# Optimization experiments

Measured on AMD Instinct MI355X. Metric: run time of the kernel, lower is better.

The kernel has to match this reference:

```python
import jax, jax.numpy as jnp
import numpy as np

SCALE = 1.0 / np.sqrt(64.0)  # hard-coded 64**0.5 in original, independent of dims


def setup_inputs() -> dict:
    key = jax.random.key(0)
    k1, k2 = jax.random.split(key)
    x = jax.random.normal(k1, (8, 2048, 1024), dtype=jnp.float32)
    # kernel[0]=W_Q, kernel[1]=W_K, kernel[2]=W_V, each [d_in, d_out]
    kernel = jax.random.normal(k2, (3, 1024, 1024), dtype=jnp.float32) * 0.02
    return {"x": x, "kernel": kernel}


def reference(x, kernel):
    # x: [b, s, d_in], kernel: [3, d_in, d_out]
    wq = jnp.einsum('bsd,de->bse', x, kernel[0])
    wk = jnp.einsum('bsd,de->bse', x, kernel[1])
    wv = jnp.einsum('bsd,de->bse', x, kernel[2])
    scores = jnp.einsum('bqe,bke->bqk', wq, wk) * SCALE  # [b, s, s]
    attn = jax.nn.softmax(scores, axis=-1)
    return jnp.einsum('bqk,bke->bqe', attn, wv)  # [b, s, d_out]
```

## Files before the change

kernel.cpp:

```cpp
#include <hip/hip_runtime.h>
#include <stdint.h>

typedef unsigned short u16;
typedef unsigned short u16x4 __attribute__((ext_vector_type(4)));
typedef unsigned short u16x8 __attribute__((ext_vector_type(8)));
typedef _Float16 f16x8 __attribute__((ext_vector_type(8)));
typedef float f32x4 __attribute__((ext_vector_type(4)));

__device__ __forceinline__ u16 f2h(float f) {
  _Float16 x = (_Float16)f;
  return __builtin_bit_cast(u16, x);
}

__device__ __forceinline__ void gld16(const void* g, void* l) {
  __builtin_amdgcn_global_load_lds(
      (const __attribute__((address_space(1))) unsigned int*)g,
      (__attribute__((address_space(3))) unsigned int*)l,
      16, 0, 0);
}

#define BAR __builtin_amdgcn_s_barrier()
#define SCHEDB __builtin_amdgcn_sched_barrier(0)
#define LGKM0                                        \
  do {                                               \
    asm volatile("s_waitcnt lgkmcnt(0)" ::: "memory"); \
    __builtin_amdgcn_sched_barrier(0);               \
  } while (0)
#define LGKM8 asm volatile("s_waitcnt lgkmcnt(8)" ::: "memory")
#define VM6 asm volatile("s_waitcnt vmcnt(6)" ::: "memory")
#define VM0 asm volatile("s_waitcnt vmcnt(0)" ::: "memory")

#define TBM 256
#define TBN 256
#define TBK 64

template <int QM, int QN>
__device__ __forceinline__ void mfma_quad(f32x4 (&acc)[8][4],
                                          const f16x8 (&ar)[4][2],
                                          const f16x8 (&br)[2][2]) {
#pragma unroll
  for (int kk = 0; kk < 2; ++kk)
#pragma unroll
    for (int mm = 0; mm < 4; ++mm)
#pragma unroll
      for (int nn = 0; nn < 2; ++nn)
        acc[QM * 4 + mm][QN * 2 + nn] = __builtin_amdgcn_mfma_f32_16x16x32_f16(
            ar[mm][kk], br[nn][kk], acc[QM * 4 + mm][QN * 2 + nn], 0, 0, 0);
}

template <int EPI, int XSWZ>
__global__ __launch_bounds__(512, 2) void gemm256(
    const u16* __restrict__ Ap, const u16* __restrict__ Bp,
    void* __restrict__ Cp, float* __restrict__ xtra, int K, int lda, int ldb,
    int ldc, long sA, long sB, long sC) {
  __shared__ char lds[131072];

  const int gx = gridDim.x, gy = gridDim.y;
  int bx, by, z;
  if constexpr (XSWZ == 1) {
    const int p = (blockIdx.z * gy + blockIdx.y) * gx + blockIdx.x;
    z = p & 7;
    const int rest = p >> 3;
    bx = rest % gx;
    by = rest / gx;
  } else {
    const int lin = (blockIdx.z * gy + blockIdx.y) * gx + blockIdx.x;
    const int cpx = (gx * gy * gridDim.z) >> 3;
    const int swz = (lin & 7) * cpx + (lin >> 3);
    bx = swz % gx;
    const int tq = swz / gx;
    by = tq % gy;
    z = tq / gy;
  }

  const int tid = threadIdx.x;
  const int lane = tid & 63, wid = tid >> 6;
  const int wr = wid >> 2, wc = wid & 3;
  const int l15 = lane & 15, l4 = lane >> 4;
  const int bm = by * TBM, bn = bx * TBN;

  const u16* Ag = Ap + (long)z * sA + (long)bm * lda;
  const u16* Bg = Bp + (long)z * sB + (long)bn * ldb;

  const int sw = l15 & 7;
  const int s0 = (l4 ^ sw) * 16, s1 = ((4 + l4) ^ sw) * 16;
  int aB[2][2], bB[2][2];
  aB[0][0] = wr * 16384 + l15 * 128 + s0;
  aB[0][1] = wr * 16384 + l15 * 128 + s1;
  bB[0][0] = 32768 + (wc >> 1) * 16384 + ((wc & 1) * 64 + l15) * 128 + s0;
  bB[0][1] = 32768 + (wc >> 1) * 16384 + ((wc & 1) * 64 + l15) * 128 + s1;
  aB[1][0] = aB[0][0] + 65536;
  aB[1][1] = aB[0][1] + 65536;
  bB[1][0] = bB[0][0] + 65536;
  bB[1][1] = bB[0][1] + 65536;

#define DSA(BUF, QM, AR)                                                     \
  do {                                                                       \
    _Pragma("unroll") for (int mm = 0; mm < 4; ++mm) {                       \
      AR[mm][0] = *(const f16x8*)(lds + aB[BUF][0] + (QM)*8192 + mm * 2048); \
      AR[mm][1] = *(const f16x8*)(lds + aB[BUF][1] + (QM)*8192 + mm * 2048); \
    }                                                                        \
  } while (0)
#define DSB(BUF, QN, BR)                                                     \
  do {                                                                       \
    _Pragma("unroll") for (int nn = 0; nn < 2; ++nn) {                       \
      BR[nn][0] = *(const f16x8*)(lds + bB[BUF][0] + (QN)*4096 + nn * 2048); \
      BR[nn][1] = *(const f16x8*)(lds + bB[BUF][1] + (QN)*4096 + nn * 2048); \
    }                                                                        \
  } while (0)

  const u16 *gpA0[2], *gpA1[2], *gpB0[2], *gpB1[2];
  int loA0[2], loA1[2], loB0[2], loB1[2];
  {
    const u16* bases[4] = {Ag, Ag + 128L * lda, Bg, Bg + 128L * ldb};
    const int lds_[4] = {lda, lda, ldb, ldb};
    const u16** gps[4] = {gpA0, gpA1, gpB0, gpB1};
    int* los[4] = {loA0, loA1, loB0, loB1};
#pragma unroll
    for (int X = 0; X < 4; ++X)
#pragma unroll
      for (int it = 0; it < 2; ++it) {
        int idx = it * 512 + tid, r = idx >> 3, p = idx & 7, s = p ^ (r & 7);
        gps[X][it] = bases[X] + (long)r * lds_[X] + s * 8;
        los[X][it] = X * 16384 + (it * 512 + wid * 64) * 16;
      }
  }
#define STAGE(X, BUF, kt)                                              \
  do {                                                                 \
    long ko = (long)(kt) << 7;                                         \
    gld16((const char*)gp##X[0] + ko, lds + ((BUF)*65536 + lo##X[0])); \
    gld16((const char*)gp##X[1] + ko, lds + ((BUF)*65536 + lo##X[1])); \
  } while (0)

  f32x4 acc[8][4] = {};
  f16x8 a0[4][2], a1[4][2], b0[2][2], b1[2][2];
  const int nk = K / TBK;

  STAGE(A0, 0, 0);
  STAGE(A1, 0, 0);
  STAGE(B0, 0, 0);
  STAGE(B1, 0, 0);
  STAGE(A0, 1, 1);
  STAGE(A1, 1, 1);
  STAGE(B0, 1, 1);
  VM6;
  BAR;
  SCHEDB;

#define TILE(BUF, t)                                                 \
  do {                                                               \
                       \
    DSA(BUF, 0, a0);                                                 \
    DSB(BUF, 0, b0);                                                 \
    if ((t) + 1 < nk) STAGE(B1, BUF ^ 1, (t) + 1);                   \
    LGKM8;                                                           \
    BAR;                                                             \
    LGKM0;                                                           \
    __builtin_amdgcn_s_setprio(1);                                   \
    mfma_quad<0, 0>(acc, a0, b0);                                    \
    __builtin_amdgcn_s_setprio(0);                                   \
    SCHEDB;                                                          \
    BAR;                                                             \
                           \
    DSA(BUF, 1, a1);                                                 \
    if ((t) + 2 < nk) STAGE(A0, BUF, (t) + 2);                       \
    BAR;                                                             \
    LGKM0;                                                           \
    __builtin_amdgcn_s_setprio(1);                                   \
    mfma_quad<1, 0>(acc, a1, b0);                                    \
    __builtin_amdgcn_s_setprio(0);                                   \
    SCHEDB;                                                          \
    BAR;                                                             \
                           \
    DSB(BUF, 1, b1);                                                 \
    if ((t) + 2 < nk) STAGE(A1, BUF, (t) + 2);                       \
    BAR;                                                             \
    LGKM0;                                                           \
    __builtin_amdgcn_s_setprio(1);                                   \
    mfma_quad<0, 1>(acc, a0, b1);                                    \
    __builtin_amdgcn_s_setprio(0);                                   \
    SCHEDB;                                                          \
    BAR;                                                             \
     \
    if ((t) + 2 < nk) {                                              \
      STAGE(B0, BUF, (t) + 2);                                       \
      VM6;                                                           \
    } else if ((t) + 1 < nk) {                                       \
      VM0;                                                           \
    }                                                                \
    BAR;                                                             \
    __builtin_amdgcn_s_setprio(1);                                   \
    mfma_quad<1, 1>(acc, a1, b1);                                    \
    __builtin_amdgcn_s_setprio(0);                                   \
    SCHEDB;                                                          \
    BAR;                                                             \
  } while (0)

  for (int t = 0; t < nk; t += 2) {
    TILE(0, t);
    TILE(1, t + 1);
  }

  if constexpr (EPI == 0) {
    if (bn < 2048) {
      u16* C = (u16*)Cp;
#pragma unroll
      for (int m = 0; m < 8; ++m)
#pragma unroll
        for (int n = 0; n < 4; ++n) {
          int row = bm + wr * 128 + m * 16 + l4 * 4;
          int col = bn + wc * 64 + n * 16 + l15;
#pragma unroll
          for (int r = 0; r < 4; ++r)
            C[(long)(row + r) * ldc + col] = f2h(acc[m][n][r]);
        }
    } else {
#pragma unroll
      for (int m = 0; m < 8; ++m) {
        const int slotk = wr * 16 + m * 2 + (l4 >> 1);
        const int koff8 = (l4 & 1) * 8;
#pragma unroll
        for (int n = 0; n < 4; ++n) {
          const int e = wc * 64 + n * 16 + l15;
          u16x4 pk;
#pragma unroll
          for (int rr = 0; rr < 4; ++rr) pk[rr] = f2h(acc[m][n][rr]);
          *(u16x4*)(lds + e * 512 + ((slotk ^ (e & 31)) << 4) + koff8) = pk;
        }
      }
      __syncthreads();
      u16* Vt = (u16*)xtra;
      const int zz = bm >> 11;
      const int kb = bm & 2047;
      const int e = tid >> 1;
      const int c2 = (tid & 1) * 16;
      u16* dst = Vt + (long)zz * 2097152 + (long)((bn - 2048) + e) * 2048 + kb;
      const char* src = lds + e * 512;
      const int ex = e & 31;
#pragma unroll
      for (int j = 0; j < 16; ++j) {
        const int c = c2 + j;
        u16x8 v = *(const u16x8*)(src + ((c ^ ex) << 4));
        *(u16x8*)(dst + c * 8) = v;
      }
    }
  } else if constexpr (EPI == 1) {
    u16* C = (u16*)Cp + (long)z * sC;
    float* rp = (float*)lds;
#pragma unroll
    for (int m = 0; m < 8; ++m) {
#pragma unroll
      for (int r = 0; r < 4; ++r) {
        const int row = bm + wr * 128 + m * 16 + l4 * 4 + r;
        float ps = 0.f;
#pragma unroll
        for (int n = 0; n < 4; ++n) {
          float p = __expf(acc[m][n][r] * 0.125f - 3.0f);
          C[(long)row * ldc + bn + wc * 64 + n * 16 + l15] = f2h(p);
          ps += p;
        }
#pragma unroll
        for (int d = 1; d < 16; d <<= 1) ps += __shfl_xor(ps, d, 64);
        if (l15 == 0) rp[wc * 256 + wr * 128 + m * 16 + l4 * 4 + r] = ps;
      }
    }
    __syncthreads();
    if (tid < 256) {
      float s = rp[tid] + rp[256 + tid] + rp[512 + tid] + rp[768 + tid];
      xtra[((long)z * 2048 + bm + tid) * 8 + bx] = s;
    }
  } else {
    float* C = (float*)Cp + (long)z * sC;
    float* ivl = (float*)lds;
    if (tid < 256) ivl[tid] = xtra[(long)z * 2048 + bm + tid];
    __syncthreads();
#pragma unroll
    for (int m = 0; m < 8; ++m)
#pragma unroll
      for (int r = 0; r < 4; ++r) {
        const int rloc = wr * 128 + m * 16 + l4 * 4 + r;
        const float iv = ivl[rloc];
        const long row = bm + rloc;
#pragma unroll
        for (int n = 0; n < 4; ++n)
          C[row * ldc + bn + wc * 64 + n * 16 + l15] = acc[m][n][r] * iv;
      }
  }
#undef TILE
#undef STAGE
#undef DSA
#undef DSB
}

__global__ __launch_bounds__(256) void rowinv_k(const float* __restrict__ Spart,
                                                float* __restrict__ rowinv) {
  const int i = blockIdx.x * 256 + threadIdx.x;
  const float* p = Spart + (long)i * 8;
  float s = 0.f;
#pragma unroll
  for (int j = 0; j < 8; ++j) s += p[j];
  rowinv[i] = 1.0f / s;
}

__global__ __launch_bounds__(256) void transpose_f32_to_f16(
    const float* __restrict__ in, u16* __restrict__ out, int R, int C,
    int ldin, long sIn, long sOut) {
  __shared__ u16 T[64][72];
  const long bi = blockIdx.z;
  const float* ip = in + bi * sIn;
  u16* op = out + bi * sOut;
  const int r0 = blockIdx.y * 64, c0 = blockIdx.x * 64;
  const int t = threadIdx.x, c8 = t & 7, rr = t >> 3;
#pragma unroll
  for (int h = 0; h < 2; ++h) {
    const int r = rr + h * 32;
    const float* g = ip + (long)(r0 + r) * ldin + c0 + c8 * 8;
    float4 a = *(const float4*)g;
    float4 b = *(const float4*)(g + 4);
    u16x8 v;
    v[0] = f2h(a.x); v[1] = f2h(a.y); v[2] = f2h(a.z); v[3] = f2h(a.w);
    v[4] = f2h(b.x); v[5] = f2h(b.y); v[6] = f2h(b.z); v[7] = f2h(b.w);
    *(u16x8*)&T[r][c8 * 8] = v;
  }
  __syncthreads();
#pragma unroll
  for (int h = 0; h < 2; ++h) {
    const int oc = rr + h * 32;
    u16x8 v;
#pragma unroll
    for (int j = 0; j < 8; ++j) v[j] = T[c8 * 8 + j][oc];
    *(u16x8*)(op + (long)(c0 + oc) * R + r0 + c8 * 8) = v;
  }
}

__global__ __launch_bounds__(256) void f32_to_f16(const float* __restrict__ in,
                                                  u16* __restrict__ out,
                                                  long n8) {
  long i = (long)blockIdx.x * 256 + threadIdx.x;
  const long stride = (long)gridDim.x * 256;
  for (; i < n8; i += stride) {
    const float* g = in + i * 8;
    float4 a = *(const float4*)g;
    float4 b = *(const float4*)(g + 4);
    u16x8 o;
    o[0] = f2h(a.x); o[1] = f2h(a.y); o[2] = f2h(a.z); o[3] = f2h(a.w);
    o[4] = f2h(b.x); o[5] = f2h(b.y); o[6] = f2h(b.z); o[7] = f2h(b.w);
    *(u16x8*)(out + i * 8) = o;
  }
}

extern "C" void kernel_launch(void* const* d_in, const int* in_sizes, int n_in,
                              void* d_out, int out_size, void* d_ws,
                              size_t ws_size, hipStream_t stream) {
  const float* x = (const float*)d_in[0];
  const float* w = (const float*)d_in[1];
  float* out = (float*)d_out;

  u16* ws = (u16*)d_ws;
  u16* QKV = ws;
  u16* Wt = ws + 50331648L;
  float* Spart = (float*)(ws + 50331648L);
  float* rowinv = (float*)(ws + 50593792L);
  u16* Vt = ws + 53477376L;
  u16* xh = ws + 70254592L;
  u16* S = ws + 70254592L;

  f32_to_f16<<<2048, 256, 0, stream>>>(x, xh, 2097152L);

  transpose_f32_to_f16<<<dim3(16, 16, 3), 256, 0, stream>>>(
      w, Wt, 1024, 1024, 1024, 1048576L, 1048576L);

  gemm256<0, 0><<<dim3(12, 64, 1), 512, 0, stream>>>(
      xh, Wt, (void*)QKV, (float*)Vt, 1024, 1024, 1024, 3072, 0L, 0L, 0L);

  gemm256<1, 1><<<dim3(8, 8, 8), 512, 0, stream>>>(
      QKV, QKV + 1024, (void*)S, Spart, 1024, 3072, 3072, 2048, 6291456L,
      6291456L, 4194304L);

  rowinv_k<<<dim3(64), 256, 0, stream>>>(Spart, rowinv);

  gemm256<2, 1><<<dim3(4, 8, 8), 512, 0, stream>>>(
      S, Vt, (void*)out, rowinv, 2048, 2048, 2048, 1024, 4194304L, 2097152L,
      2097152L);
}
```

Measured before the change: 280.4 us.

## Merge prep kernels, fold row-inverse into final GEMM, reshape V-transpose stores

Merges the x f32-to-f16 cast and the weight transpose into one launch, and removes the separate rowinv kernel by having the final GEMM epilogue sum the eight partial row sums and take the reciprocal itself. It also changes the thread-to-data mapping of the V transpose writeback so that eight consecutive threads write contiguous 16-byte chunks of a row, giving more coalesced global stores. The aim is to cut two kernel launches and their gaps, plus improve store coalescing. In exchange, every final-GEMM block now recomputes the row inverses redundantly.

```diff
diff --git a/kernel.cpp b/kernel.cpp
--- a/kernel.cpp
+++ b/kernel.cpp
@@ -232,16 +232,21 @@
       u16* Vt = (u16*)xtra;
       const int zz = bm >> 11;
       const int kb = bm & 2047;
-      const int e = tid >> 1;
-      const int c2 = (tid & 1) * 16;
-      u16* dst = Vt + (long)zz * 2097152 + (long)((bn - 2048) + e) * 2048 + kb;
-      const char* src = lds + e * 512;
-      const int ex = e & 31;
-#pragma unroll
-      for (int j = 0; j < 16; ++j) {
-        const int c = c2 + j;
-        u16x8 v = *(const u16x8*)(src + ((c ^ ex) << 4));
-        *(u16x8*)(dst + c * 8) = v;
+      const int er = tid >> 3;
+      const int q = tid & 7;
+#pragma unroll
+      for (int p = 0; p < 4; ++p) {
+        const int e = p * 64 + er;
+        const char* src = lds + e * 512;
+        u16* dst =
+            Vt + (long)zz * 2097152 + (long)((bn - 2048) + e) * 2048 + kb;
+        const int ex = e & 31;
+#pragma unroll
+        for (int j = 0; j < 4; ++j) {
+          const int c = q + 8 * j;
+          u16x8 v = *(const u16x8*)(src + ((c ^ ex) << 4));
+          *(u16x8*)(dst + c * 8) = v;
+        }
       }
     }
   } else if constexpr (EPI == 1) {
@@ -272,7 +277,13 @@
   } else {
     float* C = (float*)Cp + (long)z * sC;
     float* ivl = (float*)lds;
-    if (tid < 256) ivl[tid] = xtra[(long)z * 2048 + bm + tid];
+    if (tid < 256) {
+      const float* sp = xtra + ((long)z * 2048 + bm + tid) * 8;
+      float s = 0.f;
+#pragma unroll
+      for (int j = 0; j < 8; ++j) s += sp[j];
+      ivl[tid] = 1.0f / s;
+    }
     __syncthreads();
 #pragma unroll
     for (int m = 0; m < 8; ++m)
@@ -292,60 +303,50 @@
 #undef DSB
 }
 
-__global__ __launch_bounds__(256) void rowinv_k(const float* __restrict__ Spart,
-                                                float* __restrict__ rowinv) {
-  const int i = blockIdx.x * 256 + threadIdx.x;
-  const float* p = Spart + (long)i * 8;
-  float s = 0.f;
-#pragma unroll
-  for (int j = 0; j < 8; ++j) s += p[j];
-  rowinv[i] = 1.0f / s;
-}
-
-__global__ __launch_bounds__(256) void transpose_f32_to_f16(
-    const float* __restrict__ in, u16* __restrict__ out, int R, int C,
-    int ldin, long sIn, long sOut) {
-  __shared__ u16 T[64][72];
-  const long bi = blockIdx.z;
-  const float* ip = in + bi * sIn;
-  u16* op = out + bi * sOut;
-  const int r0 = blockIdx.y * 64, c0 = blockIdx.x * 64;
-  const int t = threadIdx.x, c8 = t & 7, rr = t >> 3;
-#pragma unroll
-  for (int h = 0; h < 2; ++h) {
-    const int r = rr + h * 32;
-    const float* g = ip + (long)(r0 + r) * ldin + c0 + c8 * 8;
-    float4 a = *(const float4*)g;
-    float4 b = *(const float4*)(g + 4);
-    u16x8 v;
-    v[0] = f2h(a.x); v[1] = f2h(a.y); v[2] = f2h(a.z); v[3] = f2h(a.w);
-    v[4] = f2h(b.x); v[5] = f2h(b.y); v[6] = f2h(b.z); v[7] = f2h(b.w);
-    *(u16x8*)&T[r][c8 * 8] = v;
-  }
-  __syncthreads();
-#pragma unroll
-  for (int h = 0; h < 2; ++h) {
-    const int oc = rr + h * 32;
-    u16x8 v;
-#pragma unroll
-    for (int j = 0; j < 8; ++j) v[j] = T[c8 * 8 + j][oc];
-    *(u16x8*)(op + (long)(c0 + oc) * R + r0 + c8 * 8) = v;
-  }
-}
-
-__global__ __launch_bounds__(256) void f32_to_f16(const float* __restrict__ in,
-                                                  u16* __restrict__ out,
-                                                  long n8) {
-  long i = (long)blockIdx.x * 256 + threadIdx.x;
-  const long stride = (long)gridDim.x * 256;
-  for (; i < n8; i += stride) {
-    const float* g = in + i * 8;
-    float4 a = *(const float4*)g;
-    float4 b = *(const float4*)(g + 4);
-    u16x8 o;
-    o[0] = f2h(a.x); o[1] = f2h(a.y); o[2] = f2h(a.z); o[3] = f2h(a.w);
-    o[4] = f2h(b.x); o[5] = f2h(b.y); o[6] = f2h(b.z); o[7] = f2h(b.w);
-    *(u16x8*)(out + i * 8) = o;
+__global__ __launch_bounds__(256) void prep(const float* __restrict__ x,
+                                            const float* __restrict__ w,
+                                            u16* __restrict__ xh,
+                                            u16* __restrict__ Wt) {
+  const int b = blockIdx.x;
+  if (b < 768) {
+    __shared__ u16 T[64][72];
+    const int z = b >> 8, rem = b & 255, by = rem >> 4, bxx = rem & 15;
+    const float* ip = w + (long)z * 1048576;
+    u16* op = Wt + (long)z * 1048576;
+    const int r0 = by * 64, c0 = bxx * 64;
+    const int t = threadIdx.x, c8 = t & 7, rr = t >> 3;
+#pragma unroll
+    for (int h = 0; h < 2; ++h) {
+      const int r = rr + h * 32;
+      const float* g = ip + (long)(r0 + r) * 1024 + c0 + c8 * 8;
+      float4 a = *(const float4*)g;
+      float4 bb = *(const float4*)(g + 4);
+      u16x8 v;
+      v[0] = f2h(a.x); v[1] = f2h(a.y); v[2] = f2h(a.z); v[3] = f2h(a.w);
+      v[4] = f2h(bb.x); v[5] = f2h(bb.y); v[6] = f2h(bb.z); v[7] = f2h(bb.w);
+      *(u16x8*)&T[r][c8 * 8] = v;
+    }
+    __syncthreads();
+#pragma unroll
+    for (int h = 0; h < 2; ++h) {
+      const int oc = rr + h * 32;
+      u16x8 v;
+#pragma unroll
+      for (int j = 0; j < 8; ++j) v[j] = T[c8 * 8 + j][oc];
+      *(u16x8*)(op + (long)(c0 + oc) * 1024 + r0 + c8 * 8) = v;
+    }
+  } else {
+    long i = (long)(b - 768) * 256 + threadIdx.x;
+    const long stride = 2048L * 256;
+    for (; i < 2097152L; i += stride) {
+      const float* g = x + i * 8;
+      float4 a = *(const float4*)g;
+      float4 bb = *(const float4*)(g + 4);
+      u16x8 o;
+      o[0] = f2h(a.x); o[1] = f2h(a.y); o[2] = f2h(a.z); o[3] = f2h(a.w);
+      o[4] = f2h(bb.x); o[5] = f2h(bb.y); o[6] = f2h(bb.z); o[7] = f2h(bb.w);
+      *(u16x8*)(xh + i * 8) = o;
+    }
   }
 }
 
@@ -360,15 +361,11 @@
   u16* QKV = ws;
   u16* Wt = ws + 50331648L;
   float* Spart = (float*)(ws + 50331648L);
-  float* rowinv = (float*)(ws + 50593792L);
   u16* Vt = ws + 53477376L;
   u16* xh = ws + 70254592L;
   u16* S = ws + 70254592L;
 
-  f32_to_f16<<<2048, 256, 0, stream>>>(x, xh, 2097152L);
-
-  transpose_f32_to_f16<<<dim3(16, 16, 3), 256, 0, stream>>>(
-      w, Wt, 1024, 1024, 1024, 1048576L, 1048576L);
+  prep<<<dim3(2816), 256, 0, stream>>>(x, w, xh, Wt);
 
   gemm256<0, 0><<<dim3(12, 64, 1), 512, 0, stream>>>(
       xh, Wt, (void*)QKV, (float*)Vt, 1024, 1024, 1024, 3072, 0L, 0L, 0L);
@@ -377,9 +374,7 @@
       QKV, QKV + 1024, (void*)S, Spart, 1024, 3072, 3072, 2048, 6291456L,
       6291456L, 4194304L);
 
-  rowinv_k<<<dim3(64), 256, 0, stream>>>(Spart, rowinv);
-
   gemm256<2, 1><<<dim3(4, 8, 8), 512, 0, stream>>>(
-      S, Vt, (void*)out, rowinv, 2048, 2048, 2048, 1024, 4194304L, 2097152L,
+      S, Vt, (void*)out, Spart, 2048, 2048, 2048, 1024, 4194304L, 2097152L,
       2097152L);
 }
```

Result: no change. 274.9 us, median of 2 (-1.9%).
